# Kernel optimization log

Measured on AMD Instinct MI355X. Metric: run time of the kernel, lower is better.

## Reference

```python
import jax, jax.numpy as jnp
import numpy as np

N_NODES = 50000
N_EDGES = 400000
IN_DIM = 512
HID = 512
HID2 = HID // 2
OUT_DIM = 2
NUM_GRAPHS = 500


def setup_inputs() -> dict:
    key = jax.random.key(0)
    ks = jax.random.split(key, 12)
    x = jax.random.normal(ks[0], (N_NODES, IN_DIM), dtype=jnp.float32)
    edge_index = jax.random.randint(ks[1], (2, N_EDGES), 0, N_NODES, dtype=jnp.int64)
    batch = jnp.sort(jax.random.randint(ks[2], (N_NODES,), 0, NUM_GRAPHS, dtype=jnp.int64))
    def lin(k, fan_out, fan_in):
        bound = 1.0 / np.sqrt(fan_in)
        return jax.random.uniform(k, (fan_out, fan_in), jnp.float32, -bound, bound)
    # SAGEConv layer 1: lin_l (on aggregated neighbors, with bias) + lin_r (root)
    W1l = lin(ks[3], HID, IN_DIM)
    b1 = jax.random.uniform(ks[4], (HID,), jnp.float32, -1/np.sqrt(IN_DIM), 1/np.sqrt(IN_DIM))
    W1r = lin(ks[5], HID, IN_DIM)
    # SAGEConv layer 2
    W2l = lin(ks[6], HID2, HID)
    b2 = jax.random.uniform(ks[7], (HID2,), jnp.float32, -1/np.sqrt(HID), 1/np.sqrt(HID))
    W2r = lin(ks[8], HID2, HID)
    # final fc
    Wfc = lin(ks[9], OUT_DIM, HID2)
    bfc = jax.random.uniform(ks[10], (OUT_DIM,), jnp.float32, -1/np.sqrt(HID2), 1/np.sqrt(HID2))
    return {"x": x, "edge_index": edge_index, "batch": batch,
            "W1l": W1l, "b1": b1, "W1r": W1r,
            "W2l": W2l, "b2": b2, "W2r": W2r,
            "Wfc": Wfc, "bfc": bfc}


def _sage_conv(h, src, dst, Wl, bl, Wr):
    # mean-aggregate source features into target nodes, then linear + root term
    n = h.shape[0]
    agg = jax.ops.segment_sum(h[src], dst, num_segments=n)          # [N, d_in]
    deg = jax.ops.segment_sum(jnp.ones(src.shape, h.dtype), dst, num_segments=n)
    agg = agg / jnp.maximum(deg, 1.0)[:, None]
    return agg @ Wl.T + bl + h @ Wr.T


def reference(x, edge_index, batch, W1l, b1, W1r, W2l, b2, W2r, Wfc, bfc):
    src, dst = edge_index[0], edge_index[1]
    h = jax.nn.relu(_sage_conv(x, src, dst, W1l, b1, W1r))
    h = jax.nn.relu(_sage_conv(h, src, dst, W2l, b2, W2r))
    # global mean pool over graph ids
    pooled = jax.ops.segment_sum(h, batch, num_segments=NUM_GRAPHS)  # [G, HID2]
    counts = jax.ops.segment_sum(jnp.ones(batch.shape, h.dtype), batch, num_segments=NUM_GRAPHS)
    pooled = pooled / jnp.maximum(counts, 1.0)[:, None]
    logits = pooled @ Wfc.T + bfc
    return jax.nn.log_softmax(logits, axis=1)
```

## Files before the change

kernel.cpp:

```cpp
#include <hip/hip_runtime.h>
#include <cstdint>

#define N_NODES 50000
#define N_PAD 50048
#define N_EDGES 400000
#define IN_DIM 512
#define HID 512
#define HID2 256
#define NUM_GRAPHS 500
#define SCAN_BLOCKS 196

typedef unsigned short u16;
typedef short s8v __attribute__((ext_vector_type(8)));
typedef float f4v __attribute__((ext_vector_type(4)));
typedef u16 u16x8 __attribute__((ext_vector_type(8)));
typedef u16 u16x4 __attribute__((ext_vector_type(4)));

__device__ __forceinline__ u16 f2bf(float f) {
  union { float f; uint32_t u; } c;
  c.f = f;
  const uint32_t u = c.u;
  return (u16)((u + 0x7fffu + ((u >> 16) & 1u)) >> 16);
}
__device__ __forceinline__ float bf2f(u16 v) {
  union { uint32_t u; float f; } c;
  c.u = ((uint32_t)v) << 16;
  return c.f;
}

__device__ __forceinline__ void gload16(const void* g, void* l) {
  __builtin_amdgcn_global_load_lds(
      (const __attribute__((address_space(1))) void*)(uintptr_t)g,
      (__attribute__((address_space(3))) void*)(uint32_t)(uintptr_t)l, 16, 0, 0);
}

__device__ __forceinline__ int xcd_swizzle(int orig, int nwg) {
  const int q = nwg >> 3, rr = nwg & 7;
  const int xcd = orig & 7, idx = orig >> 3;
  return (xcd < rr ? xcd * (q + 1) : rr * (q + 1) + (xcd - rr) * q) + idx;
}

__global__ __launch_bounds__(256) void cvt_f32_bf16(const float* __restrict__ in,
                                                    u16* __restrict__ out, int n8) {
  const int i = blockIdx.x * 256 + threadIdx.x;
  if (i >= n8) return;
  const float4 a = ((const float4*)in)[2 * i];
  const float4 b = ((const float4*)in)[2 * i + 1];
  u16x8 o;
  o[0] = f2bf(a.x); o[1] = f2bf(a.y); o[2] = f2bf(a.z); o[3] = f2bf(a.w);
  o[4] = f2bf(b.x); o[5] = f2bf(b.y); o[6] = f2bf(b.z); o[7] = f2bf(b.w);
  ((u16x8*)out)[i] = o;
}

__global__ __launch_bounds__(256) void cvt_weights(const float* __restrict__ W1l,
                                                   const float* __restrict__ W1r,
                                                   const float* __restrict__ W2l,
                                                   const float* __restrict__ W2r,
                                                   u16* __restrict__ Wc1,
                                                   u16* __restrict__ Wc2) {
  const int i = blockIdx.x * 256 + threadIdx.x;
  const float* src;
  u16* dstp;
  int l;
  if (i < 32768)      { src = W1l; dstp = Wc1;          l = i; }
  else if (i < 65536) { src = W1r; dstp = Wc1 + 262144; l = i - 32768; }
  else if (i < 81920) { src = W2l; dstp = Wc2;          l = i - 65536; }
  else                { src = W2r; dstp = Wc2 + 131072; l = i - 81920; }
  const float4 a = ((const float4*)src)[2 * l];
  const float4 b = ((const float4*)src)[2 * l + 1];
  u16x8 o;
  o[0] = f2bf(a.x); o[1] = f2bf(a.y); o[2] = f2bf(a.z); o[3] = f2bf(a.w);
  o[4] = f2bf(b.x); o[5] = f2bf(b.y); o[6] = f2bf(b.z); o[7] = f2bf(b.w);
  ((u16x8*)dstp)[l] = o;
}

template <int K, int NXL2, int NXH>
__global__ __launch_bounds__(256) void gemm_mfma(const u16* __restrict__ A,
                                                 const u16* __restrict__ B,
                                                 u16* __restrict__ CT,
                                                 u16* __restrict__ CR,
                                                 int nwg) {
  __shared__ __align__(16) u16 As[2][128 * 32];
  __shared__ __align__(16) u16 Bs[2][128 * 32];
  const int id = xcd_swizzle(blockIdx.x, nwg);
  const int bx = id & ((1 << NXL2) - 1);
  const int by = id >> NXL2;
  const int tid = threadIdx.x;
  const int lane = tid & 63;
  const int wave = tid >> 6;
  const int wr = (wave >> 1) * 64;
  const int wc = (wave & 1) * 64;
  const int fr = lane & 15;
  const int fq = lane >> 4;
  const size_t bm = (size_t)by * 128;
  const size_t bn = (size_t)bx * 128;

  const int r0 = tid >> 2;
  const int c0 = (((tid & 3) ^ ((tid >> 3) & 3)) * 8);
  const u16* gA = A + (bm + r0) * K + c0;
  const u16* gB = B + (bn + r0) * K + c0;
  const size_t rstep = (size_t)64 * K;
  const int lofs = r0 * 32 + (tid & 3) * 8;
  constexpr int nt = K >> 5;

  auto stage = [&](int b, int kt) {
    const int k0 = kt << 5;
    gload16(gA + k0, &As[b][lofs]);
    gload16(gA + rstep + k0, &As[b][lofs + 64 * 32]);
    gload16(gB + k0, &Bs[b][lofs]);
    gload16(gB + rstep + k0, &Bs[b][lofs + 64 * 32]);
  };

  f4v acc[4][4];
#pragma unroll
  for (int m = 0; m < 4; ++m)
#pragma unroll
    for (int n = 0; n < 4; ++n)
      acc[m][n] = f4v{0.f, 0.f, 0.f, 0.f};

  const int kx = (fr >> 1) & 3;
  const int slot8 = (fq ^ kx) * 8;

  stage(0, 0);
  stage(1, 1);
  asm volatile("s_waitcnt vmcnt(4)" ::: "memory");
  __builtin_amdgcn_s_barrier();

  for (int t = 0; t < nt; ++t) {
    const u16* curA = As[t & 1];
    const u16* curB = Bs[t & 1];
    s8v af[4], bf_[4];
#pragma unroll
    for (int m = 0; m < 4; ++m)
      af[m] = *(const s8v*)(curA + (wr + m * 16 + fr) * 32 + slot8);
#pragma unroll
    for (int n = 0; n < 4; ++n)
      bf_[n] = *(const s8v*)(curB + (wc + n * 16 + fr) * 32 + slot8);
#pragma unroll
    for (int m = 0; m < 4; ++m)
#pragma unroll
      for (int n = 0; n < 4; ++n)
        acc[m][n] = __builtin_amdgcn_mfma_f32_16x16x32_bf16(bf_[n], af[m],
                                                            acc[m][n], 0, 0, 0);
    if (t == nt - 1) break;
    __builtin_amdgcn_s_barrier();
    if (t + 2 < nt) {
      stage(t & 1, t + 2);
      asm volatile("s_waitcnt vmcnt(4)" ::: "memory");
    } else {
      asm volatile("s_waitcnt vmcnt(0)" ::: "memory");
    }
    __builtin_amdgcn_s_barrier();
  }

  u16* Cb = (bx < NXH) ? CT : CR;
  constexpr int ldc = NXH * 128;
  const size_t cn0 = (size_t)(bx - (bx >= NXH ? NXH : 0)) * 128 + wc;
#pragma unroll
  for (int m = 0; m < 4; ++m) {
    const size_t row = bm + wr + m * 16 + fr;
#pragma unroll
    for (int n = 0; n < 4; ++n) {
      const size_t col = cn0 + n * 16 + fq * 4;
      u16x4 p;
#pragma unroll
      for (int i = 0; i < 4; ++i) p[i] = f2bf(acc[m][n][i]);
      *(u16x4*)(Cb + row * ldc + col) = p;
    }
  }
}

__global__ void deg_hist(const int* __restrict__ dst, int* __restrict__ degi, int nE) {
  const int e = blockIdx.x * 256 + threadIdx.x;
  if (e < nE) atomicAdd(&degi[dst[e]], 1);
}

__device__ __forceinline__ int block_scan_excl(int v, int* total_out) {
  const int lane = threadIdx.x & 63;
  const int wid = threadIdx.x >> 6;
  int s = v;
#pragma unroll
  for (int off = 1; off < 64; off <<= 1) {
    const int t = __shfl_up(s, off);
    if (lane >= off) s += t;
  }
  __shared__ int wsum[4];
  if (lane == 63) wsum[wid] = s;
  __syncthreads();
  int base = 0;
#pragma unroll
  for (int w = 0; w < 4; ++w)
    if (w < wid) base += wsum[w];
  *total_out = wsum[0] + wsum[1] + wsum[2] + wsum[3];
  return base + s - v;
}

__global__ __launch_bounds__(256) void scan_blocks(const int* __restrict__ degi,
                                                   int* __restrict__ offs,
                                                   int* __restrict__ bsum, int n) {
  const int gid = blockIdx.x * 256 + threadIdx.x;
  const int v = (gid < n) ? degi[gid] : 0;
  int total;
  const int excl = block_scan_excl(v, &total);
  if (gid < n) offs[gid] = excl;
  if (threadIdx.x == 0) bsum[blockIdx.x] = total;
}

__global__ __launch_bounds__(256) void scan_bsums(int* __restrict__ bsum, int nb) {
  const int v = (threadIdx.x < nb) ? bsum[threadIdx.x] : 0;
  int total;
  const int excl = block_scan_excl(v, &total);
  if (threadIdx.x < nb) bsum[threadIdx.x] = excl;
}

__global__ __launch_bounds__(256) void add_base(int* __restrict__ offs,
                                                const int* __restrict__ bsum,
                                                int n, int nE) {
  const int gid = blockIdx.x * 256 + threadIdx.x;
  if (gid < n) offs[gid] += bsum[blockIdx.x];
  if (gid == 0) offs[n] = nE;
}

__global__ void fill_csr(const int* __restrict__ src, const int* __restrict__ dst,
                         const int* __restrict__ offs, int* __restrict__ cursor,
                         int* __restrict__ sorted_src, int nE) {
  const int e = blockIdx.x * 256 + threadIdx.x;
  if (e < nE) {
    const int d = dst[e];
    const int pos = offs[d] + atomicAdd(&cursor[d], 1);
    sorted_src[pos] = src[e];
  }
}

template <int D>
__global__ __launch_bounds__(256) void gather_combine(
    const u16* __restrict__ t, const u16* __restrict__ r,
    const float* __restrict__ bias, const int* __restrict__ offs,
    const int* __restrict__ ssrc, u16* __restrict__ hout) {
  constexpr int LPN = D / 8;
  const int node = (int)((blockIdx.x * 256u + threadIdx.x) / LPN);
  if (node >= N_NODES) return;
  const int o = (int)(threadIdx.x % LPN) * 8;
  const int beg = offs[node], end = offs[node + 1];
  float a[8] = {0.f, 0.f, 0.f, 0.f, 0.f, 0.f, 0.f, 0.f};
  int e = beg;
  for (; e + 7 < end; e += 8) {
    u16x8 v[8];
#pragma unroll
    for (int q = 0; q < 8; ++q)
      v[q] = *(const u16x8*)(t + (size_t)ssrc[e + q] * D + o);
#pragma unroll
    for (int j = 0; j < 8; ++j)
      a[j] += ((bf2f(v[0][j]) + bf2f(v[1][j])) + (bf2f(v[2][j]) + bf2f(v[3][j]))) +
              ((bf2f(v[4][j]) + bf2f(v[5][j])) + (bf2f(v[6][j]) + bf2f(v[7][j])));
  }
  if (e + 3 < end) {
    u16x8 v[4];
#pragma unroll
    for (int q = 0; q < 4; ++q)
      v[q] = *(const u16x8*)(t + (size_t)ssrc[e + q] * D + o);
#pragma unroll
    for (int j = 0; j < 8; ++j)
      a[j] += (bf2f(v[0][j]) + bf2f(v[1][j])) + (bf2f(v[2][j]) + bf2f(v[3][j]));
    e += 4;
  }
  for (; e < end; ++e) {
    const u16x8 v0 = *(const u16x8*)(t + (size_t)ssrc[e] * D + o);
#pragma unroll
    for (int j = 0; j < 8; ++j) a[j] += bf2f(v0[j]);
  }
  const float invd = 1.0f / fmaxf((float)(end - beg), 1.0f);
  const u16x8 rv = *(const u16x8*)(r + (size_t)node * D + o);
  u16x8 ov;
#pragma unroll
  for (int j = 0; j < 8; ++j)
    ov[j] = f2bf(fmaxf(fmaf(a[j], invd, bias[o + j] + bf2f(rv[j])), 0.f));
  *(u16x8*)(hout + (size_t)node * D + o) = ov;
}

__global__ __launch_bounds__(256) void pool_final(const u16* __restrict__ h,
                                                  const int* __restrict__ batch,
                                                  const float* __restrict__ Wfc,
                                                  const float* __restrict__ bfc,
                                                  float* __restrict__ out, int nNodes) {
  const int g = blockIdx.x;
  __shared__ int sbeg, send;
  if (threadIdx.x == 0) {
    int lo = 0, hi = nNodes;
    while (lo < hi) { const int mid = (lo + hi) >> 1; if (batch[mid] < g) lo = mid + 1; else hi = mid; }
    sbeg = lo;
    hi = nNodes;
    while (lo < hi) { const int mid = (lo + hi) >> 1; if (batch[mid] < g + 1) lo = mid + 1; else hi = mid; }
    send = lo;
  }
  __syncthreads();
  const int t = threadIdx.x;
  float s = 0.f;
  for (int row = sbeg; row < send; ++row) s += bf2f(h[(size_t)row * HID2 + t]);
  const float cnt = fmaxf((float)(send - sbeg), 1.0f);
  const float p = s / cnt;
  float d0 = p * Wfc[t];
  float d1 = p * Wfc[HID2 + t];
#pragma unroll
  for (int off = 32; off > 0; off >>= 1) {
    d0 += __shfl_down(d0, off);
    d1 += __shfl_down(d1, off);
  }
  __shared__ float r0[4], r1[4];
  const int wid = t >> 6, lane = t & 63;
  if (lane == 0) { r0[wid] = d0; r1[wid] = d1; }
  __syncthreads();
  if (t == 0) {
    const float l0 = r0[0] + r0[1] + r0[2] + r0[3] + bfc[0];
    const float l1 = r1[0] + r1[1] + r1[2] + r1[3] + bfc[1];
    const float m = fmaxf(l0, l1);
    const float lse = m + logf(expf(l0 - m) + expf(l1 - m));
    out[g * 2 + 0] = l0 - lse;
    out[g * 2 + 1] = l1 - lse;
  }
}

extern "C" void kernel_launch(void* const* d_in, const int* in_sizes, int n_in,
                              void* d_out, int out_size, void* d_ws, size_t ws_size,
                              hipStream_t stream) {
  (void)in_sizes; (void)n_in; (void)out_size; (void)ws_size;
  const float* x   = (const float*)d_in[0];
  const int* eidx  = (const int*)d_in[1];
  const int* batch = (const int*)d_in[2];
  const float* W1l = (const float*)d_in[3];
  const float* b1  = (const float*)d_in[4];
  const float* W1r = (const float*)d_in[5];
  const float* W2l = (const float*)d_in[6];
  const float* b2  = (const float*)d_in[7];
  const float* W2r = (const float*)d_in[8];
  const float* Wfc = (const float*)d_in[9];
  const float* bfc = (const float*)d_in[10];
  float* out = (float*)d_out;
  const int* src = eidx;
  const int* dst = eidx + N_EDGES;

  char* ws = (char*)d_ws;
  size_t off = 0;
  auto alloc = [&](size_t bytes) {
    char* p = ws + off;
    off += (bytes + 255) & ~(size_t)255;
    return p;
  };
  u16* bufT = (u16*)alloc((size_t)N_PAD * 512 * 2);
  u16* bufR = (u16*)alloc((size_t)N_PAD * 512 * 2);
  u16* bufX = (u16*)alloc((size_t)N_PAD * 512 * 2);
  u16* h1   = (u16*)alloc((size_t)N_PAD * 512 * 2);
  u16* h2   = (u16*)alloc((size_t)N_NODES * 256 * 2);
  u16* Wc1  = (u16*)alloc((size_t)1024 * 512 * 2);
  u16* Wc2  = (u16*)alloc((size_t)512 * 512 * 2);
  int* degi   = (int*)alloc((size_t)N_NODES * 4);
  int* cursor = (int*)alloc((size_t)N_NODES * 4);
  int* offs       = (int*)alloc((size_t)(N_NODES + 1) * 4);
  int* sorted_src = (int*)alloc((size_t)N_EDGES * 4);
  int* bsum       = (int*)alloc((size_t)SCAN_BLOCKS * 4);

  hipMemsetAsync(degi, 0, 200192 + (size_t)N_NODES * 4, stream);
  deg_hist<<<(N_EDGES + 255) / 256, 256, 0, stream>>>(dst, degi, N_EDGES);
  scan_blocks<<<SCAN_BLOCKS, 256, 0, stream>>>(degi, offs, bsum, N_NODES);
  scan_bsums<<<1, 256, 0, stream>>>(bsum, SCAN_BLOCKS);
  add_base<<<SCAN_BLOCKS, 256, 0, stream>>>(offs, bsum, N_NODES, N_EDGES);
  fill_csr<<<(N_EDGES + 255) / 256, 256, 0, stream>>>(src, dst, offs, cursor,
                                                      sorted_src, N_EDGES);

  cvt_f32_bf16<<<(N_NODES * (IN_DIM / 8) + 255) / 256, 256, 0, stream>>>(
      x, bufX, N_NODES * (IN_DIM / 8));
  cvt_weights<<<384, 256, 0, stream>>>(W1l, W1r, W2l, W2r, Wc1, Wc2);

  {
    const int nwg = (N_PAD / 128) * 8;
    gemm_mfma<IN_DIM, 3, 4><<<nwg, 256, 0, stream>>>(bufX, Wc1, bufT, bufR, nwg);
  }
  gather_combine<HID><<<(N_NODES + 3) / 4, 256, 0, stream>>>(
      bufT, bufR, b1, offs, sorted_src, h1);

  {
    const int nwg = (N_PAD / 128) * 4;
    gemm_mfma<HID, 2, 2><<<nwg, 256, 0, stream>>>(h1, Wc2, bufT, bufR, nwg);
  }
  gather_combine<HID2><<<(N_NODES + 7) / 8, 256, 0, stream>>>(
      bufT, bufR, b2, offs, sorted_src, h2);

  pool_final<<<NUM_GRAPHS, 256, 0, stream>>>(h2, batch, Wfc, bfc, out, N_NODES);
}
```

Measured before the change: 345.6 us.

## Fuse conversion and degree histogram into one prep kernel; triple-buffer GEMM loads

Merges the input cast, weight cast and degree histogram into a single launch that partitions work by block index, removing two kernel launches and letting the memory-bound pieces run concurrently. The MFMA GEMM moves from double to triple LDS buffering, keeping two tiles of global loads in flight while computing. This raises LDS use per block from 32KB to 48KB, which may reduce occupancy, and relies on hard-coded block counts for the prep partition.

```diff
diff --git a/kernel.cpp b/kernel.cpp
--- a/kernel.cpp
+++ b/kernel.cpp
@@ -40,38 +40,40 @@
   return (xcd < rr ? xcd * (q + 1) : rr * (q + 1) + (xcd - rr) * q) + idx;
 }
 
-__global__ __launch_bounds__(256) void cvt_f32_bf16(const float* __restrict__ in,
-                                                    u16* __restrict__ out, int n8) {
-  const int i = blockIdx.x * 256 + threadIdx.x;
-  if (i >= n8) return;
-  const float4 a = ((const float4*)in)[2 * i];
-  const float4 b = ((const float4*)in)[2 * i + 1];
-  u16x8 o;
-  o[0] = f2bf(a.x); o[1] = f2bf(a.y); o[2] = f2bf(a.z); o[3] = f2bf(a.w);
-  o[4] = f2bf(b.x); o[5] = f2bf(b.y); o[6] = f2bf(b.z); o[7] = f2bf(b.w);
-  ((u16x8*)out)[i] = o;
-}
-
-__global__ __launch_bounds__(256) void cvt_weights(const float* __restrict__ W1l,
-                                                   const float* __restrict__ W1r,
-                                                   const float* __restrict__ W2l,
-                                                   const float* __restrict__ W2r,
-                                                   u16* __restrict__ Wc1,
-                                                   u16* __restrict__ Wc2) {
-  const int i = blockIdx.x * 256 + threadIdx.x;
-  const float* src;
-  u16* dstp;
-  int l;
-  if (i < 32768)      { src = W1l; dstp = Wc1;          l = i; }
-  else if (i < 65536) { src = W1r; dstp = Wc1 + 262144; l = i - 32768; }
-  else if (i < 81920) { src = W2l; dstp = Wc2;          l = i - 65536; }
-  else                { src = W2r; dstp = Wc2 + 131072; l = i - 81920; }
-  const float4 a = ((const float4*)src)[2 * l];
-  const float4 b = ((const float4*)src)[2 * l + 1];
-  u16x8 o;
-  o[0] = f2bf(a.x); o[1] = f2bf(a.y); o[2] = f2bf(a.z); o[3] = f2bf(a.w);
-  o[4] = f2bf(b.x); o[5] = f2bf(b.y); o[6] = f2bf(b.z); o[7] = f2bf(b.w);
-  ((u16x8*)dstp)[l] = o;
+__global__ __launch_bounds__(256) void prep_kernel(
+    const float* __restrict__ x, u16* __restrict__ bufX,
+    const float* __restrict__ W1l, const float* __restrict__ W1r,
+    const float* __restrict__ W2l, const float* __restrict__ W2r,
+    u16* __restrict__ Wc1, u16* __restrict__ Wc2,
+    const int* __restrict__ dst, int* __restrict__ degi) {
+  const int b = blockIdx.x;
+  if (b < 12500) {
+    const int i = b * 256 + threadIdx.x;
+    const float4 a = ((const float4*)x)[2 * i];
+    const float4 c = ((const float4*)x)[2 * i + 1];
+    u16x8 o;
+    o[0] = f2bf(a.x); o[1] = f2bf(a.y); o[2] = f2bf(a.z); o[3] = f2bf(a.w);
+    o[4] = f2bf(c.x); o[5] = f2bf(c.y); o[6] = f2bf(c.z); o[7] = f2bf(c.w);
+    ((u16x8*)bufX)[i] = o;
+  } else if (b < 12884) {
+    const int i = (b - 12500) * 256 + threadIdx.x;
+    const float* src;
+    u16* dstp;
+    int l;
+    if (i < 32768)      { src = W1l; dstp = Wc1;          l = i; }
+    else if (i < 65536) { src = W1r; dstp = Wc1 + 262144; l = i - 32768; }
+    else if (i < 81920) { src = W2l; dstp = Wc2;          l = i - 65536; }
+    else                { src = W2r; dstp = Wc2 + 131072; l = i - 81920; }
+    const float4 a = ((const float4*)src)[2 * l];
+    const float4 c = ((const float4*)src)[2 * l + 1];
+    u16x8 o;
+    o[0] = f2bf(a.x); o[1] = f2bf(a.y); o[2] = f2bf(a.z); o[3] = f2bf(a.w);
+    o[4] = f2bf(c.x); o[5] = f2bf(c.y); o[6] = f2bf(c.z); o[7] = f2bf(c.w);
+    ((u16x8*)dstp)[l] = o;
+  } else {
+    const int e = (b - 12884) * 256 + threadIdx.x;
+    if (e < N_EDGES) atomicAdd(&degi[dst[e]], 1);
+  }
 }
 
 template <int K, int NXL2, int NXH>
@@ -80,8 +82,8 @@
                                                  u16* __restrict__ CT,
                                                  u16* __restrict__ CR,
                                                  int nwg) {
-  __shared__ __align__(16) u16 As[2][128 * 32];
-  __shared__ __align__(16) u16 Bs[2][128 * 32];
+  __shared__ __align__(16) u16 As[3][128 * 32];
+  __shared__ __align__(16) u16 Bs[3][128 * 32];
   const int id = xcd_swizzle(blockIdx.x, nwg);
   const int bx = id & ((1 << NXL2) - 1);
   const int by = id >> NXL2;
@@ -102,6 +104,7 @@
   const size_t rstep = (size_t)64 * K;
   const int lofs = r0 * 32 + (tid & 3) * 8;
   constexpr int nt = K >> 5;
+  static_assert(nt >= 3, "3-deep pipeline needs K >= 96");
 
   auto stage = [&](int b, int kt) {
     const int k0 = kt << 5;
@@ -123,12 +126,14 @@
 
   stage(0, 0);
   stage(1, 1);
-  asm volatile("s_waitcnt vmcnt(4)" ::: "memory");
+  stage(2, 2);
+  asm volatile("s_waitcnt vmcnt(8)" ::: "memory");
   __builtin_amdgcn_s_barrier();
 
+  int cur = 0;
   for (int t = 0; t < nt; ++t) {
-    const u16* curA = As[t & 1];
-    const u16* curB = Bs[t & 1];
+    const u16* curA = As[cur];
+    const u16* curB = Bs[cur];
     s8v af[4], bf_[4];
 #pragma unroll
     for (int m = 0; m < 4; ++m)
@@ -144,13 +149,16 @@
                                                             acc[m][n], 0, 0, 0);
     if (t == nt - 1) break;
     __builtin_amdgcn_s_barrier();
-    if (t + 2 < nt) {
-      stage(t & 1, t + 2);
+    if (t + 3 < nt) {
+      stage(cur, t + 3);
+      asm volatile("s_waitcnt vmcnt(8)" ::: "memory");
+    } else if (t + 2 < nt) {
       asm volatile("s_waitcnt vmcnt(4)" ::: "memory");
     } else {
       asm volatile("s_waitcnt vmcnt(0)" ::: "memory");
     }
     __builtin_amdgcn_s_barrier();
+    cur = (cur == 2) ? 0 : cur + 1;
   }
 
   u16* Cb = (bx < NXH) ? CT : CR;
@@ -168,11 +176,6 @@
       *(u16x4*)(Cb + row * ldc + col) = p;
     }
   }
-}
-
-__global__ void deg_hist(const int* __restrict__ dst, int* __restrict__ degi, int nE) {
-  const int e = blockIdx.x * 256 + threadIdx.x;
-  if (e < nE) atomicAdd(&degi[dst[e]], 1);
 }
 
 __device__ __forceinline__ int block_scan_excl(int v, int* total_out) {
@@ -360,17 +363,15 @@
   int* bsum       = (int*)alloc((size_t)SCAN_BLOCKS * 4);
 
   hipMemsetAsync(degi, 0, 200192 + (size_t)N_NODES * 4, stream);
-  deg_hist<<<(N_EDGES + 255) / 256, 256, 0, stream>>>(dst, degi, N_EDGES);
+  prep_kernel<<<14447, 256, 0, stream>>>(x, bufX, W1l, W1r, W2l, W2r,
+                                         Wc1, Wc2, dst, degi);
+
   scan_blocks<<<SCAN_BLOCKS, 256, 0, stream>>>(degi, offs, bsum, N_NODES);
   scan_bsums<<<1, 256, 0, stream>>>(bsum, SCAN_BLOCKS);
   add_base<<<SCAN_BLOCKS, 256, 0, stream>>>(offs, bsum, N_NODES, N_EDGES);
   fill_csr<<<(N_EDGES + 255) / 256, 256, 0, stream>>>(src, dst, offs, cursor,
                                                       sorted_src, N_EDGES);
 
-  cvt_f32_bf16<<<(N_NODES * (IN_DIM / 8) + 255) / 256, 256, 0, stream>>>(
-      x, bufX, N_NODES * (IN_DIM / 8));
-  cvt_weights<<<384, 256, 0, stream>>>(W1l, W1r, W2l, W2r, Wc1, Wc2);
-
   {
     const int nwg = (N_PAD / 128) * 8;
     gemm_mfma<IN_DIM, 3, 4><<<nwg, 256, 0, stream>>>(bufX, Wc1, bufT, bufR, nwg);
```

After: 340.5 us. About the same (-1.5%).
